# Kernel optimization log

Measured on AMD Instinct MI355X. Metric: run time of the kernel, lower is better.

The kernel has to match this reference:

```python
import jax, jax.numpy as jnp
import numpy as np
from jax import lax

N_QUBITS = 4   # in_channels * kernel_size^2 = 1*2*2
N_LAYERS = 2
K = 2
STRIDE = 1


def _bshape(theta, N):
    # broadcast scalar or (N,) angle to (N, 1, 1, ..., 1) for statevector broadcasting
    return jnp.broadcast_to(theta, (N,)).reshape((N,) + (1,) * N_QUBITS)


def _rx(state, theta, w):
    # RX(theta) on wire w (axis w+1): cos(t/2) I - i sin(t/2) X
    N = state.shape[0]
    c = _bshape(jnp.cos(theta * 0.5), N)
    s = _bshape(jnp.sin(theta * 0.5), N)
    return c * state - 1j * s * jnp.flip(state, axis=w + 1)


def _rz(state, theta, w):
    # RZ(theta): phase e^{-i t/2} on |0>, e^{+i t/2} on |1> of wire w
    N = state.shape[0]
    sgn = jnp.array([-0.5, 0.5], dtype=state.real.dtype).reshape(
        (1,) * (w + 1) + (2,) + (1,) * (N_QUBITS - 1 - w))
    return state * jnp.exp(1j * (_bshape(theta, N) * sgn))


def _cnot(state, control, target):
    ca, ta = control + 1, target + 1
    s0 = jnp.take(state, 0, axis=ca)
    s1 = jnp.take(state, 1, axis=ca)
    ta2 = ta if ta < ca else ta - 1
    s1 = jnp.flip(s1, axis=ta2)
    return jnp.stack([s0, s1], axis=ca)


def _simulate(angles, params):
    # angles: (N, n_qubits) float32; params: (n_layers, n_qubits, 2)
    N = angles.shape[0]
    state = jnp.zeros((N,) + (2,) * N_QUBITS, dtype=jnp.complex64)
    state = state.at[(slice(None),) + (0,) * N_QUBITS].set(1.0)
    # AngleEmbedding: RX(x_w) on wire w
    for w in range(N_QUBITS):
        state = _rx(state, angles[:, w], w)
    # quantum_circuit_1
    for l in range(N_LAYERS):
        for w in range(N_QUBITS):
            state = _rx(state, params[l, w, 0], w)
            state = _rz(state, params[l, w, 1], w)
        for w in range(N_QUBITS - 1):
            # qml.CNOT(wires=[w+1, w]) -> control w+1, target w
            state = _cnot(state, w + 1, w)
    probs = state.real ** 2 + state.imag ** 2  # (N, 2,...,2)
    zs = []
    for w in range(N_QUBITS):
        other = tuple(a for a in range(1, N_QUBITS + 1) if a != w + 1)
        m = probs.sum(axis=other)  # (N, 2)
        zs.append(m[:, 0] - m[:, 1])
    return jnp.stack(zs, axis=1)  # (N, n_qubits)


def _forward(x, params):
    B, C, H, W = x.shape
    Ho = (H - K) // STRIDE + 1
    Wo = (W - K) // STRIDE + 1
    # (B, C*K*K, Ho, Wo); feature dim flattened channel-major (C, kh, kw),
    # matching torch.flatten(input[:, :, i:i+k, j:j+k], start_dim=1)
    patches = lax.conv_general_dilated_patches(x, (K, K), (STRIDE, STRIDE), 'VALID')
    angles = patches.transpose(0, 2, 3, 1).reshape(-1, N_QUBITS)  # (B*Ho*Wo, nq)
    z = _simulate(angles, params)  # (B*Ho*Wo, nq)
    return z.reshape(B, Ho, Wo, N_QUBITS).transpose(0, 3, 1, 2)  # (B, nq, Ho, Wo)


def setup_inputs() -> dict:
    key = jax.random.key(0)
    k1, k2 = jax.random.split(key)
    x = jax.random.uniform(k1, (32, 1, 128, 128), dtype=jnp.float32)
    params = jax.random.uniform(k2, (N_LAYERS, N_QUBITS, 2), dtype=jnp.float32)
    return {"x": x, "params": params}


def reference(x, params):
    return _forward(x, params)
```

## Files before the change

kernel.cpp:

```cpp
#include <hip/hip_runtime.h>


#define HH 128
#define WW 128
#define HO 127
#define WO 127
#define BB 32
#define JSLOTS 32

template <int M>
__device__ __forceinline__ void rx_gate(float* re, float* im, float th) {
    float s, c;
    __sincosf(th * 0.5f, &s, &c);
#pragma unroll
    for (int idx = 0; idx < 16; ++idx) {
        if (idx & M) continue;
        const int p = idx | M;
        float r0 = re[idx], i0 = im[idx], r1 = re[p], i1 = im[p];
        re[idx] = fmaf(c, r0, s * i1);
        im[idx] = fmaf(c, i0, -s * r1);
        re[p]   = fmaf(c, r1, s * i0);
        im[p]   = fmaf(c, i1, -s * r0);
    }
}

template <int M>
__device__ __forceinline__ void rz_gate(float* re, float* im, float th) {
    float sp, cp;
    __sincosf(th * 0.5f, &sp, &cp);
#pragma unroll
    for (int idx = 0; idx < 16; ++idx) {
        float r = re[idx], q = im[idx];
        if (idx & M) {
            re[idx] = fmaf(r, cp, -q * sp);
            im[idx] = fmaf(q, cp, r * sp);
        } else {
            re[idx] = fmaf(r, cp, q * sp);
            im[idx] = fmaf(q, cp, -r * sp);
        }
    }
}

template <int CM, int TM>
__device__ __forceinline__ void cnot_gate(float* re, float* im) {
#pragma unroll
    for (int idx = 0; idx < 16; ++idx) {
        if ((idx & CM) && !(idx & TM)) {
            const int p = idx | TM;
            float t;
            t = re[idx]; re[idx] = re[p]; re[p] = t;
            t = im[idx]; im[idx] = im[p]; im[p] = t;
        }
    }
}

__device__ __forceinline__ void param_circuit(float* re, float* im,
                                              const float* __restrict__ prm) {
#pragma unroll
    for (int l = 0; l < 2; ++l) {
        const float* p = prm + l * 8;
        rx_gate<8>(re, im, p[0]); rz_gate<8>(re, im, p[1]);
        rx_gate<4>(re, im, p[2]); rz_gate<4>(re, im, p[3]);
        rx_gate<2>(re, im, p[4]); rz_gate<2>(re, im, p[5]);
        rx_gate<1>(re, im, p[6]); rz_gate<1>(re, im, p[7]);
        cnot_gate<4, 8>(re, im);
        cnot_gate<2, 4>(re, im);
        cnot_gate<1, 2>(re, im);
    }
}

__global__ __launch_bounds__(384) void qconv_setup(const float* __restrict__ prm,
                                                   float* __restrict__ W) {
    __shared__ float Ur[16][16];
    __shared__ float Ui[16][16];
    const int tid = threadIdx.x;
    if (tid < 16) {
        float re[16], im[16];
#pragma unroll
        for (int k = 0; k < 16; ++k) { re[k] = (k == tid) ? 1.f : 0.f; im[k] = 0.f; }
        param_circuit(re, im, prm);
#pragma unroll
        for (int k = 0; k < 16; ++k) { Ur[k][tid] = re[k]; Ui[k][tid] = im[k]; }
    }
    __syncthreads();
    if (tid < 324) {
        const int w = tid / 81;
        int p = tid % 81;
        const int pidx = p;
        const int t3 = p % 3; p /= 3;
        const int t2 = p % 3; p /= 3;
        const int t1 = p % 3;
        const int t0 = p / 3;
        const int f = (t0 == 1 ? 8 : 0) | (t1 == 1 ? 4 : 0) |
                      (t2 == 1 ? 2 : 0) | (t3 == 1 ? 1 : 0);
        const int zbit = 8 >> w;
        float acc = 0.f;
        for (int i = 0; i < 16; ++i) {
            float pr = 1.f, pi = 0.f;
            {
                int ib;
                ib = (i >> 3) & 1;
                if (t0 == 2) { if (ib) { pr = -pr; pi = -pi; } }
                else if (t0 == 1) { float tt = pr; if (ib) { pr = -pi; pi = tt; } else { pr = pi; pi = -tt; } }
                ib = (i >> 2) & 1;
                if (t1 == 2) { if (ib) { pr = -pr; pi = -pi; } }
                else if (t1 == 1) { float tt = pr; if (ib) { pr = -pi; pi = tt; } else { pr = pi; pi = -tt; } }
                ib = (i >> 1) & 1;
                if (t2 == 2) { if (ib) { pr = -pr; pi = -pi; } }
                else if (t2 == 1) { float tt = pr; if (ib) { pr = -pi; pi = tt; } else { pr = pi; pi = -tt; } }
                ib = i & 1;
                if (t3 == 2) { if (ib) { pr = -pr; pi = -pi; } }
                else if (t3 == 1) { float tt = pr; if (ib) { pr = -pi; pi = tt; } else { pr = pi; pi = -tt; } }
            }
            const int j = i ^ f;
            float sr = 0.f, si = 0.f;
            for (int k = 0; k < 16; ++k) {
                float zk = (k & zbit) ? -1.f : 1.f;
                float ar = Ur[k][j], ai = Ui[k][j];
                float br = Ur[k][i], bi = Ui[k][i];
                sr += zk * fmaf(ar, br, ai * bi);
                si += zk * fmaf(ar, bi, -ai * br);
            }
            acc += pr * sr - pi * si;
        }
        W[pidx * 4 + w] = acc * (1.0f / 16.0f);
    }
}

__global__ __launch_bounds__(256) void qconv_eval(
    const float* __restrict__ x, const float* __restrict__ W,
    float* __restrict__ out, int total_threads) {
    __shared__ float4 sW[81];
    {
        const float4* Wv = (const float4*)W;
        for (int k = threadIdx.x; k < 81; k += 256) sW[k] = Wv[k];
    }
    __syncthreads();

    int tid = blockIdx.x * blockDim.x + threadIdx.x;
    if (tid >= total_threads) return;

    const int slot = tid % JSLOTS;
    int t = tid / JSLOTS;
    const int i = t % HO;
    const int b = t / HO;
    const int j0 = slot * 4;

    const float* row0 = x + ((size_t)b * HH + i) * WW + j0;
    const float* row1 = row0 + WW;
    const float4 v0 = *(const float4*)row0;
    const float4 v1 = *(const float4*)row1;
    const bool has5 = (j0 + 4 < WW);
    const float x04 = has5 ? row0[4] : 0.f;
    const float x14 = has5 ? row1[4] : 0.f;
    const float r0[5] = {v0.x, v0.y, v0.z, v0.w, x04};
    const float r1[5] = {v1.x, v1.y, v1.z, v1.w, x14};

    float t0v[4][3], t1v[4][3], t2v[4][3], t3v[4][3];
#pragma unroll
    for (int pp = 0; pp < 4; ++pp) {
        float s, c;
        __sincosf(r0[pp], &s, &c);     t0v[pp][0] = 1.f; t0v[pp][1] = -s; t0v[pp][2] = c;
        __sincosf(r0[pp + 1], &s, &c); t1v[pp][0] = 1.f; t1v[pp][1] = -s; t1v[pp][2] = c;
        __sincosf(r1[pp], &s, &c);     t2v[pp][0] = 1.f; t2v[pp][1] = -s; t2v[pp][2] = c;
        __sincosf(r1[pp + 1], &s, &c); t3v[pp][0] = 1.f; t3v[pp][1] = -s; t3v[pp][2] = c;
    }

    float acc[4][4];
#pragma unroll
    for (int pp = 0; pp < 4; ++pp)
#pragma unroll
        for (int w = 0; w < 4; ++w) acc[pp][w] = 0.f;

#pragma unroll
    for (int p0 = 0; p0 < 3; ++p0) {
        float g0[4];
#pragma unroll
        for (int pp = 0; pp < 4; ++pp) g0[pp] = t0v[pp][p0];
#pragma unroll
        for (int p1 = 0; p1 < 3; ++p1) {
            float g1[4];
#pragma unroll
            for (int pp = 0; pp < 4; ++pp) g1[pp] = g0[pp] * t1v[pp][p1];
#pragma unroll
            for (int p2 = 0; p2 < 3; ++p2) {
                float g2[4];
#pragma unroll
                for (int pp = 0; pp < 4; ++pp) g2[pp] = g1[pp] * t2v[pp][p2];
#pragma unroll
                for (int p3 = 0; p3 < 3; ++p3) {
                    const int p = ((p0 * 3 + p1) * 3 + p2) * 3 + p3;
                    const float4 q = sW[p];
#pragma unroll
                    for (int pp = 0; pp < 4; ++pp) {
                        const float g = g2[pp] * t3v[pp][p3];
                        acc[pp][0] = fmaf(g, q.x, acc[pp][0]);
                        acc[pp][1] = fmaf(g, q.y, acc[pp][1]);
                        acc[pp][2] = fmaf(g, q.z, acc[pp][2]);
                        acc[pp][3] = fmaf(g, q.w, acc[pp][3]);
                    }
                }
            }
        }
    }

    const int npatch = (j0 + 4 <= WO) ? 4 : (WO - j0);
    float* obase = out + (((size_t)b * 4) * HO + (size_t)i) * WO + j0;
#pragma unroll
    for (int w = 0; w < 4; ++w) {
        float* o = obase + (size_t)w * HO * WO;
        for (int pp = 0; pp < npatch; ++pp) o[pp] = acc[pp][w];
    }
}

extern "C" void kernel_launch(void* const* d_in, const int* in_sizes, int n_in,
                              void* d_out, int out_size, void* d_ws, size_t ws_size,
                              hipStream_t stream) {
    const float* x = (const float*)d_in[0];
    const float* prm = (const float*)d_in[1];
    float* out = (float*)d_out;
    float* W = (float*)d_ws;

    qconv_setup<<<1, 384, 0, stream>>>(prm, W);

    const int total_threads = BB * HO * JSLOTS;
    const int blocks = (total_threads + 255) / 256;
    qconv_eval<<<blocks, 256, 0, stream>>>(x, W, out, total_threads);
}
```

Before: 78.25 us.

## Fuse weight setup into eval kernel and recompute per block

Merges the single-block setup kernel into the evaluation kernel so every block recomputes the circuit unitary and the 81x4 weight table in shared memory. The setup is also restructured: the Z-weighted U^H U products are computed once into shared matrices and then reduced, instead of being recomputed inside each Pauli-term loop. This removes a kernel launch, the serial dependency and the workspace round trip, at the cost of redundant setup work in each block.

```diff
diff --git a/kernel.cpp b/kernel.cpp
--- a/kernel.cpp
+++ b/kernel.cpp
@@ -69,11 +69,17 @@
     }
 }
 
-__global__ __launch_bounds__(384) void qconv_setup(const float* __restrict__ prm,
-                                                   float* __restrict__ W) {
+__global__ __launch_bounds__(256) void qconv_fused(
+    const float* __restrict__ x, const float* __restrict__ prm,
+    float* __restrict__ out) {
     __shared__ float Ur[16][16];
     __shared__ float Ui[16][16];
+    __shared__ float Mr[4][16][16];
+    __shared__ float Mi[4][16][16];
+    __shared__ float4 sW[81];
+
     const int tid = threadIdx.x;
+
     if (tid < 16) {
         float re[16], im[16];
 #pragma unroll
@@ -83,36 +89,15 @@
         for (int k = 0; k < 16; ++k) { Ur[k][tid] = re[k]; Ui[k][tid] = im[k]; }
     }
     __syncthreads();
-    if (tid < 324) {
-        const int w = tid / 81;
-        int p = tid % 81;
-        const int pidx = p;
-        const int t3 = p % 3; p /= 3;
-        const int t2 = p % 3; p /= 3;
-        const int t1 = p % 3;
-        const int t0 = p / 3;
-        const int f = (t0 == 1 ? 8 : 0) | (t1 == 1 ? 4 : 0) |
-                      (t2 == 1 ? 2 : 0) | (t3 == 1 ? 1 : 0);
+
+    {
+        const int w = tid >> 6;
         const int zbit = 8 >> w;
-        float acc = 0.f;
-        for (int i = 0; i < 16; ++i) {
-            float pr = 1.f, pi = 0.f;
-            {
-                int ib;
-                ib = (i >> 3) & 1;
-                if (t0 == 2) { if (ib) { pr = -pr; pi = -pi; } }
-                else if (t0 == 1) { float tt = pr; if (ib) { pr = -pi; pi = tt; } else { pr = pi; pi = -tt; } }
-                ib = (i >> 2) & 1;
-                if (t1 == 2) { if (ib) { pr = -pr; pi = -pi; } }
-                else if (t1 == 1) { float tt = pr; if (ib) { pr = -pi; pi = tt; } else { pr = pi; pi = -tt; } }
-                ib = (i >> 1) & 1;
-                if (t2 == 2) { if (ib) { pr = -pr; pi = -pi; } }
-                else if (t2 == 1) { float tt = pr; if (ib) { pr = -pi; pi = tt; } else { pr = pi; pi = -tt; } }
-                ib = i & 1;
-                if (t3 == 2) { if (ib) { pr = -pr; pi = -pi; } }
-                else if (t3 == 1) { float tt = pr; if (ib) { pr = -pi; pi = tt; } else { pr = pi; pi = -tt; } }
-            }
-            const int j = i ^ f;
+        const int base = (tid & 63) * 4;
+#pragma unroll
+        for (int r = 0; r < 4; ++r) {
+            const int e = base + r;
+            const int j = e >> 4, i = e & 15;
             float sr = 0.f, si = 0.f;
             for (int k = 0; k < 16; ++k) {
                 float zk = (k & zbit) ? -1.f : 1.f;
@@ -121,27 +106,48 @@
                 sr += zk * fmaf(ar, br, ai * bi);
                 si += zk * fmaf(ar, bi, -ai * br);
             }
-            acc += pr * sr - pi * si;
-        }
-        W[pidx * 4 + w] = acc * (1.0f / 16.0f);
-    }
-}
-
-__global__ __launch_bounds__(256) void qconv_eval(
-    const float* __restrict__ x, const float* __restrict__ W,
-    float* __restrict__ out, int total_threads) {
-    __shared__ float4 sW[81];
-    {
-        const float4* Wv = (const float4*)W;
-        for (int k = threadIdx.x; k < 81; k += 256) sW[k] = Wv[k];
+            Mr[w][j][i] = sr;
+            Mi[w][j][i] = si;
+        }
     }
     __syncthreads();
 
-    int tid = blockIdx.x * blockDim.x + threadIdx.x;
-    if (tid >= total_threads) return;
-
-    const int slot = tid % JSLOTS;
-    int t = tid / JSLOTS;
+    for (int cc = tid; cc < 324; cc += 256) {
+        const int w = cc / 81;
+        int p = cc % 81;
+        const int pidx = p;
+        const int t3 = p % 3; p /= 3;
+        const int t2 = p % 3; p /= 3;
+        const int t1 = p % 3;
+        const int t0 = p / 3;
+        const int f = (t0 == 1 ? 8 : 0) | (t1 == 1 ? 4 : 0) |
+                      (t2 == 1 ? 2 : 0) | (t3 == 1 ? 1 : 0);
+        float acc = 0.f;
+        for (int i = 0; i < 16; ++i) {
+            float pr = 1.f, pi = 0.f;
+            int ib;
+            ib = (i >> 3) & 1;
+            if (t0 == 2) { if (ib) { pr = -pr; pi = -pi; } }
+            else if (t0 == 1) { float tt = pr; if (ib) { pr = -pi; pi = tt; } else { pr = pi; pi = -tt; } }
+            ib = (i >> 2) & 1;
+            if (t1 == 2) { if (ib) { pr = -pr; pi = -pi; } }
+            else if (t1 == 1) { float tt = pr; if (ib) { pr = -pi; pi = tt; } else { pr = pi; pi = -tt; } }
+            ib = (i >> 1) & 1;
+            if (t2 == 2) { if (ib) { pr = -pr; pi = -pi; } }
+            else if (t2 == 1) { float tt = pr; if (ib) { pr = -pi; pi = tt; } else { pr = pi; pi = -tt; } }
+            ib = i & 1;
+            if (t3 == 2) { if (ib) { pr = -pr; pi = -pi; } }
+            else if (t3 == 1) { float tt = pr; if (ib) { pr = -pi; pi = tt; } else { pr = pi; pi = -tt; } }
+            const int j = i ^ f;
+            acc += pr * Mr[w][j][i] - pi * Mi[w][j][i];
+        }
+        ((float*)sW)[pidx * 4 + w] = acc * (1.0f / 16.0f);
+    }
+    __syncthreads();
+
+    const int tid_g = blockIdx.x * blockDim.x + tid;
+    const int slot = tid_g % JSLOTS;
+    int t = tid_g / JSLOTS;
     const int i = t % HO;
     const int b = t / HO;
     const int j0 = slot * 4;
@@ -219,11 +225,8 @@
     const float* x = (const float*)d_in[0];
     const float* prm = (const float*)d_in[1];
     float* out = (float*)d_out;
-    float* W = (float*)d_ws;
-
-    qconv_setup<<<1, 384, 0, stream>>>(prm, W);
 
     const int total_threads = BB * HO * JSLOTS;
-    const int blocks = (total_threads + 255) / 256;
-    qconv_eval<<<blocks, 256, 0, stream>>>(x, W, out, total_threads);
-}
+    const int blocks = total_threads / 256;
+    qconv_fused<<<blocks, 256, 0, stream>>>(x, prm, out);
+}
```

New measurement: 70.70 us. 9.6% less time.
